# Kernel optimization log

Measured on AMD Instinct MI355X. Metric: run time of the kernel, lower is better.

The kernel has to match this reference:

```python
import jax, jax.numpy as jnp
import numpy as np

B, S, D, H, DK, F, L, V = 4, 128, 512, 8, 64, 2048, 2, 32000
N = B * S  # nodes per side (enc and dec each)


def _pe():
    pos = np.arange(S, dtype=np.float32)[:, None]
    div = np.exp(-np.log(10000.0) * np.arange(0, D, 2, dtype=np.float32) / D)
    pe = np.zeros((S, D), dtype=np.float32)
    pe[:, 0::2] = np.sin(pos * div)
    pe[:, 1::2] = np.cos(pos * div)
    return jnp.asarray(np.tile(pe, (B, 1)))  # [N, D]


def _ln(x, g, b, eps=1e-5):
    mu = jnp.mean(x, -1, keepdims=True)
    var = jnp.mean(jnp.square(x - mu), -1, keepdims=True)
    return g * (x - mu) * jax.lax.rsqrt(var + eps) + b


def _edge_attn(q, k, v, src, dst, n_dst):
    # src_dot_dst('k','q','score') then scaled_exp, then src_mul_edge + sum scatter
    s = jnp.sum(k[src] * q[dst], -1, keepdims=True) / np.float32(np.sqrt(DK))  # [E,H,1]
    s = jnp.exp(jnp.clip(s, -10.0, 10.0))
    wv = jax.ops.segment_sum(v[src] * s, dst, num_segments=n_dst)  # [n_dst,H,DK]
    z = jax.ops.segment_sum(s, dst, num_segments=n_dst)            # [n_dst,H,1]
    return wv / z


def _attn_block(x_q, x_kv, Wq, Wk, Wv, Wo, src, dst):
    q = (x_q @ Wq).reshape(-1, H, DK)
    k = (x_kv @ Wk).reshape(-1, H, DK)
    v = (x_kv @ Wv).reshape(-1, H, DK)
    o = _edge_attn(q, k, v, src, dst, x_q.shape[0]).reshape(-1, D)
    return o @ Wo


def _forward(p, src_tok, tgt_tok, ee_src, ee_dst, dd_src, dd_dst, ed_src, ed_dst):
    (src_emb, tgt_emb, enc_Wqkv, enc_Wo, enc_ln1, enc_W1, enc_b1, enc_W2, enc_b2,
     enc_ln2, enc_lnf, dec_Wqkv, dec_Wo, dec_ln1, dec_cWq, dec_cWkv, dec_cWo,
     dec_ln2, dec_W1, dec_b1, dec_W2, dec_b2, dec_ln3, dec_lnf, gen_W, gen_b) = p
    pe = _pe()
    scale = np.float32(np.sqrt(D))
    x_e = src_emb[src_tok].reshape(N, D) * scale + pe  # token + positional embed
    x_d = tgt_emb[tgt_tok].reshape(N, D) * scale + pe
    for l in range(L):  # encoder layers (ee edges)
        xn = _ln(x_e, enc_ln1[l, 0], enc_ln1[l, 1])
        x_e = x_e + _attn_block(xn, xn, enc_Wqkv[l, 0], enc_Wqkv[l, 1], enc_Wqkv[l, 2], enc_Wo[l], ee_src, ee_dst)
        xn = _ln(x_e, enc_ln2[l, 0], enc_ln2[l, 1])
        x_e = x_e + jax.nn.relu(xn @ enc_W1[l] + enc_b1[l]) @ enc_W2[l] + enc_b2[l]
    x_e = _ln(x_e, enc_lnf[0], enc_lnf[1])
    for l in range(L):  # decoder layers: self (dd) then cross (ed)
        xn = _ln(x_d, dec_ln1[l, 0], dec_ln1[l, 1])
        x_d = x_d + _attn_block(xn, xn, dec_Wqkv[l, 0], dec_Wqkv[l, 1], dec_Wqkv[l, 2], dec_Wo[l], dd_src, dd_dst)
        xn = _ln(x_d, dec_ln2[l, 0], dec_ln2[l, 1])
        x_d = x_d + _attn_block(xn, x_e, dec_cWq[l], dec_cWkv[l, 0], dec_cWkv[l, 1], dec_cWo[l], ed_src, ed_dst)
        xn = _ln(x_d, dec_ln3[l, 0], dec_ln3[l, 1])
        x_d = x_d + jax.nn.relu(xn @ dec_W1[l] + dec_b1[l]) @ dec_W2[l] + dec_b2[l]
    x_d = _ln(x_d, dec_lnf[0], dec_lnf[1])
    return jax.nn.log_softmax(x_d @ gen_W + gen_b, axis=-1)  # generator


def setup_inputs():
    key = jax.random.key(0)
    ks = iter(jax.random.split(key, 32))
    w = lambda *shape: jax.random.normal(next(ks), shape, jnp.float32) * 0.02
    lnp = lambda n: jnp.tile(jnp.stack([jnp.ones(D), jnp.zeros(D)])[None], (n, 1, 1))
    # structured edge lists: per-sentence blocks
    i, j = np.meshgrid(np.arange(S), np.arange(S), indexing='ij')  # src pos, dst pos
    base = (np.arange(B)[:, None] * S).astype(np.int32)
    full_s = (base + i.ravel()[None, :]).ravel().astype(np.int32)
    full_d = (base + j.ravel()[None, :]).ravel().astype(np.int32)
    m = i.ravel() <= j.ravel()  # causal mask for dec self-attention
    dd_s = (base + i.ravel()[m][None, :]).ravel().astype(np.int32)
    dd_d = (base + j.ravel()[m][None, :]).ravel().astype(np.int32)
    k1, k2 = jax.random.split(next(ks))
    return dict(
        src_emb=w(V, D), tgt_emb=w(V, D),
        enc_Wqkv=w(L, 3, D, D), enc_Wo=w(L, D, D), enc_ln1=lnp(L),
        enc_W1=w(L, D, F), enc_b1=jnp.zeros((L, F)), enc_W2=w(L, F, D),
        enc_b2=jnp.zeros((L, D)), enc_ln2=lnp(L), enc_lnf=lnp(1)[0],
        dec_Wqkv=w(L, 3, D, D), dec_Wo=w(L, D, D), dec_ln1=lnp(L),
        dec_cWq=w(L, D, D), dec_cWkv=w(L, 2, D, D), dec_cWo=w(L, D, D), dec_ln2=lnp(L),
        dec_W1=w(L, D, F), dec_b1=jnp.zeros((L, F)), dec_W2=w(L, F, D),
        dec_b2=jnp.zeros((L, D)), dec_ln3=lnp(L), dec_lnf=lnp(1)[0],
        gen_W=w(D, V), gen_b=jnp.zeros((V,)),
        src_tok=jax.random.randint(k1, (B, S), 0, V, jnp.int32),
        tgt_tok=jax.random.randint(k2, (B, S), 0, V, jnp.int32),
        ee_src=jnp.asarray(full_s), ee_dst=jnp.asarray(full_d),
        dd_src=jnp.asarray(dd_s), dd_dst=jnp.asarray(dd_d),
        ed_src=jnp.asarray(full_s), ed_dst=jnp.asarray(full_d),
    )


def reference(src_emb, tgt_emb, enc_Wqkv, enc_Wo, enc_ln1, enc_W1, enc_b1, enc_W2,
              enc_b2, enc_ln2, enc_lnf, dec_Wqkv, dec_Wo, dec_ln1, dec_cWq,
              dec_cWkv, dec_cWo, dec_ln2, dec_W1, dec_b1, dec_W2, dec_b2,
              dec_ln3, dec_lnf, gen_W, gen_b, src_tok, tgt_tok, ee_src, ee_dst,
              dd_src, dd_dst, ed_src, ed_dst):
    p = (src_emb, tgt_emb, enc_Wqkv, enc_Wo, enc_ln1, enc_W1, enc_b1, enc_W2,
         enc_b2, enc_ln2, enc_lnf, dec_Wqkv, dec_Wo, dec_ln1, dec_cWq, dec_cWkv,
         dec_cWo, dec_ln2, dec_W1, dec_b1, dec_W2, dec_b2, dec_ln3, dec_lnf,
         gen_W, gen_b)
    return _forward(p, src_tok, tgt_tok, ee_src, ee_dst, dd_src, dd_dst, ed_src, ed_dst)
```

## Files before the change

### kernel.cpp

```cpp
#include <hip/hip_runtime.h>
#include <cstddef>

constexpr int cB = 4, cS = 128, cD = 512, cH = 8, cDK = 64, cF = 2048, cL = 2, cV = 32000;
constexpr int cN = cB * cS;

typedef __attribute__((ext_vector_type(8)))  short short8;
typedef __attribute__((ext_vector_type(4)))  float f32x4;
typedef __attribute__((ext_vector_type(16))) float f32x16;

__device__ __forceinline__ short f2bf(float x) {
    unsigned u = __builtin_bit_cast(unsigned, x);
    unsigned r = (u + 0x7fffu + ((u >> 16) & 1u)) >> 16;
    return (short)r;
}
__device__ __forceinline__ short f2h(float x) {
    return __builtin_bit_cast(short, (_Float16)x);
}
__device__ __forceinline__ float h2f(short s) {
    return (float)__builtin_bit_cast(_Float16, s);
}

__device__ __forceinline__ void bar_lgkm() {
    asm volatile("s_waitcnt lgkmcnt(0)" ::: "memory");
    __builtin_amdgcn_s_barrier();
    asm volatile("" ::: "memory");
}

__global__ __launch_bounds__(256) void embed_k(const float* __restrict__ e0,
                                               const int* __restrict__ t0,
                                               float* __restrict__ X0,
                                               const float* __restrict__ e1,
                                               const int* __restrict__ t1,
                                               float* __restrict__ X1)
{
    const float* emb = blockIdx.z ? e1 : e0;
    const int* tok   = blockIdx.z ? t1 : t0;
    float* X         = blockIdx.z ? X1 : X0;
    int n = blockIdx.x;
    int tid = threadIdx.x;
    int t = tok[n];
    int pos = n & (cS - 1);
    const float scale = 22.62741699796952f;
    for (int d = tid; d < cD; d += 256) {
        int i2 = d & ~1;
        float div = expf(-9.210340371976184f * (float)i2 / (float)cD);
        float arg = (float)pos * div;
        float p = (d & 1) ? cosf(arg) : sinf(arg);
        X[(long)n * cD + d] = emb[(long)t * cD + d] * scale + p;
    }
}

__global__ __launch_bounds__(256) void ln_k(const float* __restrict__ X,
                                            const float* __restrict__ g,
                                            const float* __restrict__ bta,
                                            short* __restrict__ Yb)
{
    __shared__ float red[256];
    int row = blockIdx.x, tid = threadIdx.x;
    const float* x = X + (long)row * cD;
    float v0 = x[tid], v1 = x[tid + 256];

    red[tid] = v0 + v1;
    __syncthreads();
    for (int st = 128; st > 0; st >>= 1) { if (tid < st) red[tid] += red[tid + st]; __syncthreads(); }
    float mu = red[0] * (1.0f / (float)cD);
    __syncthreads();

    float d0 = v0 - mu, d1 = v1 - mu;
    red[tid] = d0 * d0 + d1 * d1;
    __syncthreads();
    for (int st = 128; st > 0; st >>= 1) { if (tid < st) red[tid] += red[tid + st]; __syncthreads(); }
    float var = red[0] * (1.0f / (float)cD);
    float rs = rsqrtf(var + 1e-5f);

    Yb[(long)row * cD + tid]       = f2bf(g[tid]       * d0 * rs + bta[tid]);
    Yb[(long)row * cD + tid + 256] = f2bf(g[tid + 256] * d1 * rs + bta[tid + 256]);
}

struct TCP { const float* s[24]; };

__global__ __launch_bounds__(256) void tconv_k(TCP ptrs, short* __restrict__ dst,
                                               int K, int N)
{
    __shared__ float t[64][65];
    const float* s = ptrs.s[blockIdx.z];
    short* d = dst + (long)blockIdx.z * K * N;
    int k0 = blockIdx.y * 64, n0 = blockIdx.x * 64;
    int tid = threadIdx.x;
    const f32x4* s4 = (const f32x4*)s;
#pragma unroll
    for (int i = 0; i < 4; i++) {
        int lin = tid + i * 256;
        int r = lin >> 4, c4 = lin & 15;
        f32x4 v = s4[(long)(k0 + r) * (N >> 2) + (n0 >> 2) + c4];
        t[r][c4 * 4 + 0] = v[0]; t[r][c4 * 4 + 1] = v[1];
        t[r][c4 * 4 + 2] = v[2]; t[r][c4 * 4 + 3] = v[3];
    }
    __syncthreads();
#pragma unroll
    for (int i = 0; i < 2; i++) {
        int lin = tid + i * 256;
        int r = lin >> 3, c8 = lin & 7;
        short8 o;
#pragma unroll
        for (int j = 0; j < 8; j++) o[j] = f2bf(t[c8 * 8 + j][r]);
        *(short8*)&d[(long)(n0 + r) * K + k0 + c8 * 8] = o;
    }
}

template <int MR, int NR, bool LNF>
__global__ __launch_bounds__(256) void gemm_k(
    const short* __restrict__ Abf, const float* __restrict__ Af,
    const float* __restrict__ lng, const float* __restrict__ lnb,
    const short* __restrict__ Bt,
    const float* __restrict__ bias, const float* __restrict__ res,
    float* __restrict__ C, short* __restrict__ Cb,
    int N, int K, int relu, long btStride, long cStride, int swz)
{
    constexpr int BM = MR * 32, BN = NR * 32, BK = 64, PITCH = BK + 8;
    constexpr int ACH = (BM * BK) / (8 * 256);
    constexpr int BCH = (BN * BK) / (8 * 256);
    static_assert(ACH >= 1 && BCH >= 1, "tile too small");
    __shared__ short As[2][BM * PITCH];
    __shared__ short Bs[2][BN * PITCH];
    __shared__ float mu_s[BM], rs_s[BM];
    __shared__ float gb_s[2][512];

    int bx = blockIdx.x, by = blockIdx.y;
    if (swz) {
        int nb = gridDim.x * gridDim.y;
        int bid = by * gridDim.x + bx;
        int w = (bid & 7) * (nb >> 3) + (bid >> 3);
        by = w % gridDim.y; bx = w / gridDim.y;
    }

    const short* Bm = Bt + (long)blockIdx.z * btStride;
    int tid = threadIdx.x;
    int lane = tid & 63, wid = tid >> 6;
    int wr = wid >> 1, wc = wid & 1;
    int m0 = by * BM, n0 = bx * BN;
    int lrow = lane & 15, koff = (lane >> 4) * 8;

    f32x4 acc[MR][NR];
#pragma unroll
    for (int m = 0; m < MR; m++)
#pragma unroll
        for (int n = 0; n < NR; n++) acc[m][n] = f32x4{0.f, 0.f, 0.f, 0.f};

    short8 qa0[ACH], qa1[ACH], qb0[BCH], qb1[BCH];
    f32x4 fa0[LNF ? ACH * 2 : 1], fa1[LNF ? ACH * 2 : 1];

    auto stageA = [&](int k0, short8 (&qa)[ACH], f32x4 (&fa)[LNF ? ACH * 2 : 1]) {
#pragma unroll
        for (int i = 0; i < ACH; i++) {
            int lin = tid + i * 256, r = lin >> 3, c8 = lin & 7;
            if constexpr (LNF) {
                const f32x4* p = (const f32x4*)(Af + (long)(m0 + r) * K + k0 + c8 * 8);
                fa[2 * i] = p[0]; fa[2 * i + 1] = p[1];
            } else {
                qa[i] = *(const short8*)&Abf[(long)(m0 + r) * K + k0 + c8 * 8];
            }
        }
    };
    auto stageB = [&](int k0, short8 (&qb)[BCH]) {
#pragma unroll
        for (int i = 0; i < BCH; i++) {
            int lin = tid + i * 256, r = lin >> 3, c8 = lin & 7;
            qb[i] = *(const short8*)&Bm[(long)(n0 + r) * K + k0 + c8 * 8];
        }
    };
    auto writeT = [&](int buf, int k0, short8 (&qa)[ACH],
                      f32x4 (&fa)[LNF ? ACH * 2 : 1], short8 (&qb)[BCH]) {
#pragma unroll
        for (int i = 0; i < ACH; i++) {
            int lin = tid + i * 256, r = lin >> 3, c8 = lin & 7;
            if constexpr (LNF) {
                float mu = mu_s[r], rs = rs_s[r];
                short8 o;
#pragma unroll
                for (int j = 0; j < 4; j++)
                    o[j] = f2bf((fa[2 * i][j] - mu) * rs * gb_s[0][k0 + c8 * 8 + j] + gb_s[1][k0 + c8 * 8 + j]);
#pragma unroll
                for (int j = 0; j < 4; j++)
                    o[4 + j] = f2bf((fa[2 * i + 1][j] - mu) * rs * gb_s[0][k0 + c8 * 8 + 4 + j] + gb_s[1][k0 + c8 * 8 + 4 + j]);
                *(short8*)&As[buf][r * PITCH + c8 * 8] = o;
            } else {
                *(short8*)&As[buf][r * PITCH + c8 * 8] = qa[i];
            }
        }
#pragma unroll
        for (int i = 0; i < BCH; i++) {
            int lin = tid + i * 256, r = lin >> 3, c8 = lin & 7;
            *(short8*)&Bs[buf][r * PITCH + c8 * 8] = qb[i];
        }
    };
    auto mfmaStep = [&](int buf) {
#pragma unroll
        for (int kk = 0; kk < BK; kk += 32) {
            short8 a[MR], b[NR];
#pragma unroll
            for (int m = 0; m < MR; m++)
                a[m] = *(const short8*)&As[buf][(wr * MR * 16 + m * 16 + lrow) * PITCH + kk + koff];
#pragma unroll
            for (int n = 0; n < NR; n++)
                b[n] = *(const short8*)&Bs[buf][(wc * NR * 16 + n * 16 + lrow) * PITCH + kk + koff];
#pragma unroll
            for (int m = 0; m < MR; m++)
#pragma unroll
                for (int n = 0; n < NR; n++)
                    acc[m][n] = __builtin_amdgcn_mfma_f32_16x16x32_bf16(a[m], b[n], acc[m][n], 0, 0, 0);
        }
    };

    stageA(0, qa0, fa0); stageB(0, qb0);
    if (BK < K) { stageA(BK, qa1, fa1); stageB(BK, qb1); }

    if constexpr (LNF) {
        constexpr int TPR = 256 / BM;
        int r = tid / TPR, sub = tid % TPR;
        const f32x4* row4 = (const f32x4*)(Af + (long)(m0 + r) * K);
        float s = 0.f, s2 = 0.f;
        for (int i = sub; i < (K >> 2); i += TPR) {
            f32x4 v = row4[i];
            s  += v[0] + v[1] + v[2] + v[3];
            s2 += v[0] * v[0] + v[1] * v[1] + v[2] * v[2] + v[3] * v[3];
        }
#pragma unroll
        for (int o = TPR >> 1; o > 0; o >>= 1) {
            s += __shfl_xor(s, o); s2 += __shfl_xor(s2, o);
        }
        if (sub == 0) {
            float mu = s / (float)K;
            float var = s2 / (float)K - mu * mu;
            mu_s[r] = mu; rs_s[r] = rsqrtf(var + 1e-5f);
        }
        for (int i = tid; i < 512; i += 256) {
            gb_s[0][i] = lng[i]; gb_s[1][i] = lnb[i];
        }
        bar_lgkm();
    }

    int k0 = 0;
    for (;;) {
        writeT(0, k0, qa0, fa0, qb0);
        if (k0 + 2 * BK < K) { stageA(k0 + 2 * BK, qa0, fa0); stageB(k0 + 2 * BK, qb0); }
        bar_lgkm();
        mfmaStep(0);
        k0 += BK; if (k0 >= K) break;

        writeT(1, k0, qa1, fa1, qb1);
        if (k0 + 2 * BK < K) { stageA(k0 + 2 * BK, qa1, fa1); stageB(k0 + 2 * BK, qb1); }
        bar_lgkm();
        mfmaStep(1);
        k0 += BK; if (k0 >= K) break;
    }

#pragma unroll
    for (int m = 0; m < MR; m++) {
        int rbase = m0 + wr * MR * 16 + m * 16 + (lane >> 4) * 4;
#pragma unroll
        for (int n = 0; n < NR; n++) {
            int col = n0 + wc * NR * 16 + n * 16 + (lane & 15);
            float bv = bias ? bias[col] : 0.f;
#pragma unroll
            for (int j = 0; j < 4; j++) {
                long row = rbase + j;
                float v = acc[m][n][j] + bv;
                if (res)  v += res[row * N + col];
                if (relu) v = fmaxf(v, 0.f);
                long off = row * N + col + (long)blockIdx.z * cStride;
                if (C)  C[off] = v;
                if (Cb) Cb[off] = f2bf(v);
            }
        }
    }
}

__global__ __launch_bounds__(256) void attn_k(const short* __restrict__ Q,
                                              const short* __restrict__ Km,
                                              const short* __restrict__ Vm,
                                              short* __restrict__ O, int causal)
{
    __shared__ short q_s[64 * 72];
    __shared__ short k_s[128 * 72];
    __shared__ short vt_s[64 * 128];
    __shared__ short p_s[64 * 136];
    __shared__ float z_s[64];

    int tid = threadIdx.x, lane = tid & 63, wid = tid >> 6;
    int lr = lane & 15, lg = lane >> 4;
    int h = blockIdx.x, b = blockIdx.y, dstBase = blockIdx.z * 64;
    const int RS = cH * cDK;
    long qbase = ((long)b * cS + dstBase) * RS + h * cDK;
    long kbase = ((long)b * cS) * RS + h * cDK;

#pragma unroll
    for (int i = 0; i < 2; i++) {
        int lin = tid + i * 256, t = lin >> 3, c8 = lin & 7;
        *(short8*)&q_s[t * 72 + c8 * 8] = *(const short8*)&Q[qbase + (long)t * RS + c8 * 8];
    }
#pragma unroll
    for (int i = 0; i < 4; i++) {
        int lin = tid + i * 256, t = lin >> 3, c8 = lin & 7;
        *(short8*)&k_s[t * 72 + c8 * 8] = *(const short8*)&Km[kbase + (long)t * RS + c8 * 8];
    }
#pragma unroll
    for (int i = 0; i < 4; i++) {
        int lin = tid + i * 256, src = lin >> 3, c8 = lin & 7;
        short8 v = *(const short8*)&Vm[kbase + (long)src * RS + c8 * 8];
#pragma unroll
        for (int j = 0; j < 8; j++) {
            int dk = c8 * 8 + j;
            int g = (src >> 3) ^ (dk >> 3);
            vt_s[dk * 128 + g * 8 + (src & 7)] = v[j];
        }
    }
    bar_lgkm();

    f32x4 sacc[8];
#pragma unroll
    for (int n = 0; n < 8; n++) sacc[n] = f32x4{0.f, 0.f, 0.f, 0.f};
#pragma unroll
    for (int kk = 0; kk < 64; kk += 32) {
        short8 a = *(const short8*)&q_s[(wid * 16 + lr) * 72 + kk + lg * 8];
#pragma unroll
        for (int n = 0; n < 8; n++) {
            short8 bf = *(const short8*)&k_s[(n * 16 + lr) * 72 + kk + lg * 8];
            sacc[n] = __builtin_amdgcn_mfma_f32_16x16x32_bf16(a, bf, sacc[n], 0, 0, 0);
        }
    }
    float z[4] = {0.f, 0.f, 0.f, 0.f};
#pragma unroll
    for (int n = 0; n < 8; n++) {
        int src = n * 16 + lr;
#pragma unroll
        for (int j = 0; j < 4; j++) {
            int dst = dstBase + wid * 16 + lg * 4 + j;
            float s = sacc[n][j] * 0.125f;
            s = __expf(fminf(fmaxf(s, -10.f), 10.f));
            if (causal && src > dst) s = 0.f;
            sacc[n][j] = s;
            z[j] += s;
        }
    }
#pragma unroll
    for (int j = 0; j < 4; j++) {
        z[j] += __shfl_xor(z[j], 1); z[j] += __shfl_xor(z[j], 2);
        z[j] += __shfl_xor(z[j], 4); z[j] += __shfl_xor(z[j], 8);
    }
#pragma unroll
    for (int n = 0; n < 8; n++) {
        int src = n * 16 + lr;
#pragma unroll
        for (int j = 0; j < 4; j++)
            p_s[(wid * 16 + lg * 4 + j) * 136 + src] = f2bf(sacc[n][j]);
    }
    if (lr == 0) {
#pragma unroll
        for (int j = 0; j < 4; j++) z_s[wid * 16 + lg * 4 + j] = z[j];
    }
    bar_lgkm();

    f32x4 oacc[4];
#pragma unroll
    for (int n = 0; n < 4; n++) oacc[n] = f32x4{0.f, 0.f, 0.f, 0.f};
#pragma unroll
    for (int kk = 0; kk < 128; kk += 32) {
        int dkr = wid * 16 + lr;
        int g = ((kk >> 3) + lg) ^ (dkr >> 3);
        short8 a = *(const short8*)&vt_s[dkr * 128 + g * 8];
#pragma unroll
        for (int n = 0; n < 4; n++) {
            short8 bf = *(const short8*)&p_s[(n * 16 + lr) * 136 + kk + lg * 8];
            oacc[n] = __builtin_amdgcn_mfma_f32_16x16x32_bf16(a, bf, oacc[n], 0, 0, 0);
        }
    }
#pragma unroll
    for (int n = 0; n < 4; n++) {
        int dl = n * 16 + lr;
        float zz = z_s[dl];
#pragma unroll
        for (int j = 0; j < 4; j++) {
            int dk = wid * 16 + lg * 4 + j;
            O[qbase + (long)dl * RS + dk] = f2bf(oacc[n][j] / zz);
        }
    }
}

__global__ __launch_bounds__(256) void gen32_k(
    const short* __restrict__ A, const short* __restrict__ Bt,
    const float* __restrict__ bias, short* __restrict__ Ch, int N, int K)
{
    constexpr int PITCH = 72;
    constexpr int ACH = 4, BCH = 4;
    __shared__ short As[2][128 * PITCH];
    __shared__ short Bs[2][128 * PITCH];

    int bx = blockIdx.x, by = blockIdx.y;
    {
        int nb = gridDim.x * gridDim.y;
        int bid = by * gridDim.x + bx;
        int w = (bid & 7) * (nb >> 3) + (bid >> 3);
        by = w % gridDim.y; bx = w / gridDim.y;
    }
    int tid = threadIdx.x;
    int lane = tid & 63, wid = tid >> 6;
    int wr = wid >> 1, wc = wid & 1;
    int m0 = by * 128, n0 = bx * 128;
    int l31 = lane & 31, l5 = lane >> 5;

    f32x16 acc[2][2];
#pragma unroll
    for (int m = 0; m < 2; m++)
#pragma unroll
        for (int n = 0; n < 2; n++)
#pragma unroll
            for (int r = 0; r < 16; r++) acc[m][n][r] = 0.f;

    short8 qa0[ACH], qa1[ACH], qb0[BCH], qb1[BCH];
    auto stage = [&](int k0, short8 (&qa)[ACH], short8 (&qb)[BCH]) {
#pragma unroll
        for (int i = 0; i < ACH; i++) {
            int lin = tid + i * 256, r = lin >> 3, c8 = lin & 7;
            qa[i] = *(const short8*)&A[(long)(m0 + r) * K + k0 + c8 * 8];
        }
#pragma unroll
        for (int i = 0; i < BCH; i++) {
            int lin = tid + i * 256, r = lin >> 3, c8 = lin & 7;
            qb[i] = *(const short8*)&Bt[(long)(n0 + r) * K + k0 + c8 * 8];
        }
    };
    auto writeT = [&](int buf, short8 (&qa)[ACH], short8 (&qb)[BCH]) {
#pragma unroll
        for (int i = 0; i < ACH; i++) {
            int lin = tid + i * 256, r = lin >> 3, c8 = lin & 7;
            *(short8*)&As[buf][r * PITCH + c8 * 8] = qa[i];
        }
#pragma unroll
        for (int i = 0; i < BCH; i++) {
            int lin = tid + i * 256, r = lin >> 3, c8 = lin & 7;
            *(short8*)&Bs[buf][r * PITCH + c8 * 8] = qb[i];
        }
    };
    auto mfmaStep = [&](int buf) {
#pragma unroll
        for (int kk = 0; kk < 64; kk += 16) {
            short8 a[2], b[2];
#pragma unroll
            for (int m = 0; m < 2; m++)
                a[m] = *(const short8*)&As[buf][(wr * 64 + m * 32 + l31) * PITCH + kk + l5 * 8];
#pragma unroll
            for (int n = 0; n < 2; n++)
                b[n] = *(const short8*)&Bs[buf][(wc * 64 + n * 32 + l31) * PITCH + kk + l5 * 8];
#pragma unroll
            for (int m = 0; m < 2; m++)
#pragma unroll
                for (int n = 0; n < 2; n++)
                    acc[m][n] = __builtin_amdgcn_mfma_f32_32x32x16_bf16(a[m], b[n], acc[m][n], 0, 0, 0);
        }
    };

    const int steps = K >> 6;
    stage(0, qa0, qb0);
    stage(64, qa1, qb1);
    int st = 0;
    for (;;) {
        writeT(0, qa0, qb0);
        if (st + 2 < steps) stage((st + 2) * 64, qa0, qb0);
        bar_lgkm();
        mfmaStep(0);
        st++; if (st >= steps) break;

        writeT(1, qa1, qb1);
        if (st + 2 < steps) stage((st + 2) * 64, qa1, qb1);
        bar_lgkm();
        mfmaStep(1);
        st++; if (st >= steps) break;
    }

#pragma unroll
    for (int m = 0; m < 2; m++) {
#pragma unroll
        for (int n = 0; n < 2; n++) {
            int col = n0 + wc * 64 + n * 32 + l31;
            float bv = bias[col];
#pragma unroll
            for (int r = 0; r < 16; r++) {
                int row = m0 + wr * 64 + m * 32 + (r & 3) + 8 * (r >> 2) + 4 * l5;
                Ch[(long)row * N + col] = f2h(acc[m][n][r] + bv);
            }
        }
    }
}

__global__ __launch_bounds__(256) void lsm_k(const short* __restrict__ L16,
                                             float* __restrict__ Out)
{
    __shared__ float rm[256], rs[256];
    int row = blockIdx.x, tid = threadIdx.x;
    const short8* x8 = (const short8*)(L16 + (long)row * cV);
    float* o = Out + (long)row * cV;
    constexpr int NV = cV / 8;

    float m = -1e30f, s = 0.f;
    for (int i = tid; i < NV; i += 256) {
        short8 v = x8[i];
        float f[8];
#pragma unroll
        for (int j = 0; j < 8; j++) f[j] = h2f(v[j]);
        float cm = f[0];
#pragma unroll
        for (int j = 1; j < 8; j++) cm = fmaxf(cm, f[j]);
        float nm = fmaxf(m, cm);
        float a = 0.f;
#pragma unroll
        for (int j = 0; j < 8; j++) a += __expf(f[j] - nm);
        s = s * __expf(m - nm) + a;
        m = nm;
    }
    rm[tid] = m; rs[tid] = s;
    __syncthreads();
    for (int st = 128; st > 0; st >>= 1) {
        if (tid < st) {
            float m2 = rm[tid + st], s2 = rs[tid + st];
            float nm = fmaxf(rm[tid], m2);
            rs[tid] = rs[tid] * __expf(rm[tid] - nm) + s2 * __expf(m2 - nm);
            rm[tid] = nm;
        }
        __syncthreads();
    }
    float lse = rm[0] + __logf(rs[0]);

    for (int i = tid; i < NV; i += 256) {
        short8 v = x8[i];
        f32x4 o0, o1;
#pragma unroll
        for (int j = 0; j < 4; j++) o0[j] = h2f(v[j]) - lse;
#pragma unroll
        for (int j = 0; j < 4; j++) o1[j] = h2f(v[4 + j]) - lse;
        *(f32x4*)&o[i * 8]     = o0;
        *(f32x4*)&o[i * 8 + 4] = o1;
    }
}

extern "C" void kernel_launch(void* const* d_in, const int* in_sizes, int n_in,
                              void* d_out, int out_size, void* d_ws, size_t ws_size,
                              hipStream_t stream)
{
    const float* src_emb  = (const float*)d_in[0];
    const float* tgt_emb  = (const float*)d_in[1];
    const float* enc_Wqkv = (const float*)d_in[2];
    const float* enc_Wo   = (const float*)d_in[3];
    const float* enc_ln1  = (const float*)d_in[4];
    const float* enc_W1   = (const float*)d_in[5];
    const float* enc_b1   = (const float*)d_in[6];
    const float* enc_W2   = (const float*)d_in[7];
    const float* enc_b2   = (const float*)d_in[8];
    const float* enc_ln2  = (const float*)d_in[9];
    const float* enc_lnf  = (const float*)d_in[10];
    const float* dec_Wqkv = (const float*)d_in[11];
    const float* dec_Wo   = (const float*)d_in[12];
    const float* dec_ln1  = (const float*)d_in[13];
    const float* dec_cWq  = (const float*)d_in[14];
    const float* dec_cWkv = (const float*)d_in[15];
    const float* dec_cWo  = (const float*)d_in[16];
    const float* dec_ln2  = (const float*)d_in[17];
    const float* dec_W1   = (const float*)d_in[18];
    const float* dec_b1   = (const float*)d_in[19];
    const float* dec_W2   = (const float*)d_in[20];
    const float* dec_b2   = (const float*)d_in[21];
    const float* dec_ln3  = (const float*)d_in[22];
    const float* dec_lnf  = (const float*)d_in[23];
    const float* gen_W    = (const float*)d_in[24];
    const float* gen_b    = (const float*)d_in[25];
    const int* src_tok    = (const int*)d_in[26];
    const int* tgt_tok    = (const int*)d_in[27];

    const long ND = (long)cN * cD;
    const long DD = (long)cD * cD;
    const long DF = (long)cD * cF;

    float* x_e = (float*)d_ws;
    float* x_d = x_e + ND;

    short* qkvb  = (short*)(x_d + ND);
    short* ob_bf = qkvb + 3 * ND;
    short* hb_bf = ob_bf + ND;
    short* kvc   = hb_bf + (long)cN * cF;
    short* xn_bf = kvc + 4 * ND;
    short* wDD  = xn_bf + ND;
    short* wDF  = wDD + 24 * DD;
    short* wFD  = wDF + 4 * DF;
    short* genT = wFD + 4 * DF;
    short* lg16 = genT + (long)cD * cV;

    {
        TCP p{};
        int i = 0;
        for (int j = 0; j < 6; j++) p.s[i++] = enc_Wqkv + (long)j * DD;
        for (int j = 0; j < 2; j++) p.s[i++] = enc_Wo   + (long)j * DD;
        for (int j = 0; j < 6; j++) p.s[i++] = dec_Wqkv + (long)j * DD;
        for (int j = 0; j < 2; j++) p.s[i++] = dec_Wo   + (long)j * DD;
        for (int j = 0; j < 2; j++) p.s[i++] = dec_cWq  + (long)j * DD;
        for (int j = 0; j < 4; j++) p.s[i++] = dec_cWkv + (long)j * DD;
        for (int j = 0; j < 2; j++) p.s[i++] = dec_cWo  + (long)j * DD;
        tconv_k<<<dim3(cD / 64, cD / 64, 24), 256, 0, stream>>>(p, wDD, cD, cD);
    }
    {
        TCP p{};
        p.s[0] = enc_W1; p.s[1] = enc_W1 + DF; p.s[2] = dec_W1; p.s[3] = dec_W1 + DF;
        tconv_k<<<dim3(cF / 64, cD / 64, 4), 256, 0, stream>>>(p, wDF, cD, cF);
    }
    {
        TCP p{};
        p.s[0] = enc_W2; p.s[1] = enc_W2 + DF; p.s[2] = dec_W2; p.s[3] = dec_W2 + DF;
        tconv_k<<<dim3(cD / 64, cF / 64, 4), 256, 0, stream>>>(p, wFD, cF, cD);
    }
    {
        TCP p{};
        p.s[0] = gen_W;
        tconv_k<<<dim3(cV / 64, cD / 64, 1), 256, 0, stream>>>(p, genT, cD, cV);
    }

    embed_k<<<dim3(cN, 1, 2), 256, 0, stream>>>(src_emb, src_tok, x_e,
                                                tgt_emb, tgt_tok, x_d);

    dim3 gDD(cD / 32, cN / 32);
    dim3 gFFN1(cF / 64, cN / 64);
    dim3 gAttn(cH, cB, 2);

    for (int l = 0; l < cL; l++) {
        gemm_k<1, 1, true><<<dim3(cD / 32, cN / 32, 3), 256, 0, stream>>>(
            nullptr, x_e, enc_ln1 + (long)(2 * l) * cD, enc_ln1 + (long)(2 * l + 1) * cD,
            wDD + (long)(3 * l) * DD, nullptr, nullptr, nullptr, qkvb,
            cD, cD, 0, DD, ND, 0);
        attn_k<<<gAttn, 256, 0, stream>>>(qkvb, qkvb + ND, qkvb + 2 * ND, ob_bf, 0);
        gemm_k<1, 1, false><<<gDD, 256, 0, stream>>>(
            ob_bf, nullptr, nullptr, nullptr, wDD + (long)(6 + l) * DD,
            nullptr, x_e, x_e, nullptr, cD, cD, 0, 0, 0, 0);
        gemm_k<2, 2, true><<<gFFN1, 256, 0, stream>>>(
            nullptr, x_e, enc_ln2 + (long)(2 * l) * cD, enc_ln2 + (long)(2 * l + 1) * cD,
            wDF + (long)l * DF, enc_b1 + (long)l * cF, nullptr, nullptr, hb_bf,
            cF, cD, 1, 0, 0, 0);
        gemm_k<1, 1, false><<<gDD, 256, 0, stream>>>(
            hb_bf, nullptr, nullptr, nullptr, wFD + (long)l * DF,
            enc_b2 + (long)l * cD, x_e, x_e, nullptr, cD, cF, 0, 0, 0, 0);
    }

    gemm_k<1, 1, true><<<dim3(cD / 32, cN / 32, 4), 256, 0, stream>>>(
        nullptr, x_e, enc_lnf, enc_lnf + cD,
        wDD + 18 * DD, nullptr, nullptr, nullptr, kvc, cD, cD, 0, DD, ND, 0);

    for (int l = 0; l < cL; l++) {
        gemm_k<1, 1, true><<<dim3(cD / 32, cN / 32, 3), 256, 0, stream>>>(
            nullptr, x_d, dec_ln1 + (long)(2 * l) * cD, dec_ln1 + (long)(2 * l + 1) * cD,
            wDD + (long)(8 + 3 * l) * DD, nullptr, nullptr, nullptr, qkvb,
            cD, cD, 0, DD, ND, 0);
        attn_k<<<gAttn, 256, 0, stream>>>(qkvb, qkvb + ND, qkvb + 2 * ND, ob_bf, 1);
        gemm_k<1, 1, false><<<gDD, 256, 0, stream>>>(
            ob_bf, nullptr, nullptr, nullptr, wDD + (long)(14 + l) * DD,
            nullptr, x_d, x_d, nullptr, cD, cD, 0, 0, 0, 0);

        gemm_k<1, 1, true><<<gDD, 256, 0, stream>>>(
            nullptr, x_d, dec_ln2 + (long)(2 * l) * cD, dec_ln2 + (long)(2 * l + 1) * cD,
            wDD + (long)(16 + l) * DD, nullptr, nullptr, nullptr, qkvb,
            cD, cD, 0, 0, 0, 0);
        attn_k<<<gAttn, 256, 0, stream>>>(qkvb, kvc + (long)(2 * l) * ND,
                                          kvc + (long)(2 * l + 1) * ND, ob_bf, 0);
        gemm_k<1, 1, false><<<gDD, 256, 0, stream>>>(
            ob_bf, nullptr, nullptr, nullptr, wDD + (long)(22 + l) * DD,
            nullptr, x_d, x_d, nullptr, cD, cD, 0, 0, 0, 0);

        gemm_k<2, 2, true><<<gFFN1, 256, 0, stream>>>(
            nullptr, x_d, dec_ln3 + (long)(2 * l) * cD, dec_ln3 + (long)(2 * l + 1) * cD,
            wDF + (long)(2 + l) * DF, dec_b1 + (long)l * cF, nullptr, nullptr, hb_bf,
            cF, cD, 1, 0, 0, 0);
        gemm_k<1, 1, false><<<gDD, 256, 0, stream>>>(
            hb_bf, nullptr, nullptr, nullptr, wFD + (long)(2 + l) * DF,
            dec_b2 + (long)l * cD, x_d, x_d, nullptr, cD, cF, 0, 0, 0, 0);
    }

    ln_k<<<cN, 256, 0, stream>>>(x_d, dec_lnf, dec_lnf + cD, xn_bf);
    gen32_k<<<dim3(cV / 128, cN / 128), 256, 0, stream>>>(
        xn_bf, genT, gen_b, lg16, cV, cD);
    lsm_k<<<cN, 256, 0, stream>>>(lg16, (float*)d_out);
}
```

Before: 357.0 us.

## Split K across two warp groups in 512-thread GEMM with shared-memory reduction

Replaces the 256-thread layer GEMM with a 512-thread variant in which two groups of four warps each handle half of the K dimension, staging 128-wide K slices. The two partial accumulators are combined through shared memory before the epilogue. LayerNorm normalisation now happens in registers when the tile is staged rather than when it is written to LDS, and the grid swizzle option is removed. The vocabulary GEMM also drops from a K tile of 64 to 32, which halves its LDS footprint but doubles its barrier steps. The aim is more warps per block to hide latency on these small GEMMs, at the cost of an extra reduction pass and more barriers.

```diff
diff --git a/kernel.cpp b/kernel.cpp
--- a/kernel.cpp
+++ b/kernel.cpp
@@ -109,114 +109,35 @@
 }
 
 template <int MR, int NR, bool LNF>
-__global__ __launch_bounds__(256) void gemm_k(
+__global__ __launch_bounds__(512) void gemm8_k(
     const short* __restrict__ Abf, const float* __restrict__ Af,
     const float* __restrict__ lng, const float* __restrict__ lnb,
     const short* __restrict__ Bt,
     const float* __restrict__ bias, const float* __restrict__ res,
     float* __restrict__ C, short* __restrict__ Cb,
-    int N, int K, int relu, long btStride, long cStride, int swz)
-{
-    constexpr int BM = MR * 32, BN = NR * 32, BK = 64, PITCH = BK + 8;
-    constexpr int ACH = (BM * BK) / (8 * 256);
-    constexpr int BCH = (BN * BK) / (8 * 256);
+    int N, int K, int relu, long btStride, long cStride)
+{
+    constexpr int BM = MR * 32, BN = NR * 32, PITCH = 136;
+    constexpr int ACH = (BM * 128) / (8 * 512);
+    constexpr int BCH = (BN * 128) / (8 * 512);
     static_assert(ACH >= 1 && BCH >= 1, "tile too small");
     __shared__ short As[2][BM * PITCH];
     __shared__ short Bs[2][BN * PITCH];
+    __shared__ float red[4][64][MR * NR * 4];
     __shared__ float mu_s[BM], rs_s[BM];
-    __shared__ float gb_s[2][512];
-
-    int bx = blockIdx.x, by = blockIdx.y;
-    if (swz) {
-        int nb = gridDim.x * gridDim.y;
-        int bid = by * gridDim.x + bx;
-        int w = (bid & 7) * (nb >> 3) + (bid >> 3);
-        by = w % gridDim.y; bx = w / gridDim.y;
-    }
+    __shared__ float gb_s[2][LNF ? 512 : 8];
 
     const short* Bm = Bt + (long)blockIdx.z * btStride;
     int tid = threadIdx.x;
     int lane = tid & 63, wid = tid >> 6;
-    int wr = wid >> 1, wc = wid & 1;
-    int m0 = by * BM, n0 = bx * BN;
+    int grp = wid >> 2, quad = wid & 3;
+    int wr = quad >> 1, wc = quad & 1;
+    int m0 = blockIdx.y * BM, n0 = blockIdx.x * BN;
     int lrow = lane & 15, koff = (lane >> 4) * 8;
-
-    f32x4 acc[MR][NR];
-#pragma unroll
-    for (int m = 0; m < MR; m++)
-#pragma unroll
-        for (int n = 0; n < NR; n++) acc[m][n] = f32x4{0.f, 0.f, 0.f, 0.f};
-
-    short8 qa0[ACH], qa1[ACH], qb0[BCH], qb1[BCH];
-    f32x4 fa0[LNF ? ACH * 2 : 1], fa1[LNF ? ACH * 2 : 1];
-
-    auto stageA = [&](int k0, short8 (&qa)[ACH], f32x4 (&fa)[LNF ? ACH * 2 : 1]) {
-#pragma unroll
-        for (int i = 0; i < ACH; i++) {
-            int lin = tid + i * 256, r = lin >> 3, c8 = lin & 7;
-            if constexpr (LNF) {
-                const f32x4* p = (const f32x4*)(Af + (long)(m0 + r) * K + k0 + c8 * 8);
-                fa[2 * i] = p[0]; fa[2 * i + 1] = p[1];
-            } else {
-                qa[i] = *(const short8*)&Abf[(long)(m0 + r) * K + k0 + c8 * 8];
-            }
-        }
-    };
-    auto stageB = [&](int k0, short8 (&qb)[BCH]) {
-#pragma unroll
-        for (int i = 0; i < BCH; i++) {
-            int lin = tid + i * 256, r = lin >> 3, c8 = lin & 7;
-            qb[i] = *(const short8*)&Bm[(long)(n0 + r) * K + k0 + c8 * 8];
-        }
-    };
-    auto writeT = [&](int buf, int k0, short8 (&qa)[ACH],
-                      f32x4 (&fa)[LNF ? ACH * 2 : 1], short8 (&qb)[BCH]) {
-#pragma unroll
-        for (int i = 0; i < ACH; i++) {
-            int lin = tid + i * 256, r = lin >> 3, c8 = lin & 7;
-            if constexpr (LNF) {
-                float mu = mu_s[r], rs = rs_s[r];
-                short8 o;
-#pragma unroll
-                for (int j = 0; j < 4; j++)
-                    o[j] = f2bf((fa[2 * i][j] - mu) * rs * gb_s[0][k0 + c8 * 8 + j] + gb_s[1][k0 + c8 * 8 + j]);
-#pragma unroll
-                for (int j = 0; j < 4; j++)
-                    o[4 + j] = f2bf((fa[2 * i + 1][j] - mu) * rs * gb_s[0][k0 + c8 * 8 + 4 + j] + gb_s[1][k0 + c8 * 8 + 4 + j]);
-                *(short8*)&As[buf][r * PITCH + c8 * 8] = o;
-            } else {
-                *(short8*)&As[buf][r * PITCH + c8 * 8] = qa[i];
-            }
-        }
-#pragma unroll
-        for (int i = 0; i < BCH; i++) {
-            int lin = tid + i * 256, r = lin >> 3, c8 = lin & 7;
-            *(short8*)&Bs[buf][r * PITCH + c8 * 8] = qb[i];
-        }
-    };
-    auto mfmaStep = [&](int buf) {
-#pragma unroll
-        for (int kk = 0; kk < BK; kk += 32) {
-            short8 a[MR], b[NR];
-#pragma unroll
-            for (int m = 0; m < MR; m++)
-                a[m] = *(const short8*)&As[buf][(wr * MR * 16 + m * 16 + lrow) * PITCH + kk + koff];
-#pragma unroll
-            for (int n = 0; n < NR; n++)
-                b[n] = *(const short8*)&Bs[buf][(wc * NR * 16 + n * 16 + lrow) * PITCH + kk + koff];
-#pragma unroll
-            for (int m = 0; m < MR; m++)
-#pragma unroll
-                for (int n = 0; n < NR; n++)
-                    acc[m][n] = __builtin_amdgcn_mfma_f32_16x16x32_bf16(a[m], b[n], acc[m][n], 0, 0, 0);
-        }
-    };
-
-    stageA(0, qa0, fa0); stageB(0, qb0);
-    if (BK < K) { stageA(BK, qa1, fa1); stageB(BK, qb1); }
+    const int Kh = K >> 1;
 
     if constexpr (LNF) {
-        constexpr int TPR = 256 / BM;
+        constexpr int TPR = 512 / BM;
         int r = tid / TPR, sub = tid % TPR;
         const f32x4* row4 = (const f32x4*)(Af + (long)(m0 + r) * K);
         float s = 0.f, s2 = 0.f;
@@ -234,43 +155,125 @@
             float var = s2 / (float)K - mu * mu;
             mu_s[r] = mu; rs_s[r] = rsqrtf(var + 1e-5f);
         }
-        for (int i = tid; i < 512; i += 256) {
-            gb_s[0][i] = lng[i]; gb_s[1][i] = lnb[i];
-        }
+        if (tid < 512) { gb_s[0][tid] = lng[tid]; gb_s[1][tid] = lnb[tid]; }
         bar_lgkm();
     }
 
-    int k0 = 0;
+    f32x4 acc[MR][NR];
+#pragma unroll
+    for (int m = 0; m < MR; m++)
+#pragma unroll
+        for (int n = 0; n < NR; n++) acc[m][n] = f32x4{0.f, 0.f, 0.f, 0.f};
+
+    short8 qa0[ACH], qa1[ACH], qb0[BCH], qb1[BCH];
+
+    auto stage = [&](int step, short8 (&qa)[ACH], short8 (&qb)[BCH]) {
+#pragma unroll
+        for (int i = 0; i < ACH; i++) {
+            int lin = tid + i * 512, r = lin >> 4, c8 = lin & 15;
+            int kg = (c8 < 8) ? (step * 64 + c8 * 8) : (Kh + step * 64 + (c8 - 8) * 8);
+            if constexpr (LNF) {
+                const f32x4* p = (const f32x4*)(Af + (long)(m0 + r) * K + kg);
+                f32x4 f0 = p[0], f1 = p[1];
+                float mu = mu_s[r], rs = rs_s[r];
+                short8 o;
+#pragma unroll
+                for (int j = 0; j < 4; j++)
+                    o[j] = f2bf((f0[j] - mu) * rs * gb_s[0][kg + j] + gb_s[1][kg + j]);
+#pragma unroll
+                for (int j = 0; j < 4; j++)
+                    o[4 + j] = f2bf((f1[j] - mu) * rs * gb_s[0][kg + 4 + j] + gb_s[1][kg + 4 + j]);
+                qa[i] = o;
+            } else {
+                qa[i] = *(const short8*)&Abf[(long)(m0 + r) * K + kg];
+            }
+        }
+#pragma unroll
+        for (int i = 0; i < BCH; i++) {
+            int lin = tid + i * 512, r = lin >> 4, c8 = lin & 15;
+            int kg = (c8 < 8) ? (step * 64 + c8 * 8) : (Kh + step * 64 + (c8 - 8) * 8);
+            qb[i] = *(const short8*)&Bm[(long)(n0 + r) * K + kg];
+        }
+    };
+    auto writeT = [&](int buf, short8 (&qa)[ACH], short8 (&qb)[BCH]) {
+#pragma unroll
+        for (int i = 0; i < ACH; i++) {
+            int lin = tid + i * 512, r = lin >> 4, c8 = lin & 15;
+            *(short8*)&As[buf][r * PITCH + c8 * 8] = qa[i];
+        }
+#pragma unroll
+        for (int i = 0; i < BCH; i++) {
+            int lin = tid + i * 512, r = lin >> 4, c8 = lin & 15;
+            *(short8*)&Bs[buf][r * PITCH + c8 * 8] = qb[i];
+        }
+    };
+    auto mfmaStep = [&](int buf) {
+#pragma unroll
+        for (int kk2 = 0; kk2 < 2; kk2++) {
+            int kk = grp * 64 + kk2 * 32;
+            short8 a[MR], b[NR];
+#pragma unroll
+            for (int m = 0; m < MR; m++)
+                a[m] = *(const short8*)&As[buf][(wr * MR * 16 + m * 16 + lrow) * PITCH + kk + koff];
+#pragma unroll
+            for (int n = 0; n < NR; n++)
+                b[n] = *(const short8*)&Bs[buf][(wc * NR * 16 + n * 16 + lrow) * PITCH + kk + koff];
+#pragma unroll
+            for (int m = 0; m < MR; m++)
+#pragma unroll
+                for (int n = 0; n < NR; n++)
+                    acc[m][n] = __builtin_amdgcn_mfma_f32_16x16x32_bf16(a[m], b[n], acc[m][n], 0, 0, 0);
+        }
+    };
+
+    const int steps = K >> 7;
+    stage(0, qa0, qb0);
+    if (steps > 1) stage(1, qa1, qb1);
+
+    int st = 0;
     for (;;) {
-        writeT(0, k0, qa0, fa0, qb0);
-        if (k0 + 2 * BK < K) { stageA(k0 + 2 * BK, qa0, fa0); stageB(k0 + 2 * BK, qb0); }
+        writeT(0, qa0, qb0);
+        if (st + 2 < steps) stage(st + 2, qa0, qb0);
         bar_lgkm();
         mfmaStep(0);
-        k0 += BK; if (k0 >= K) break;
-
-        writeT(1, k0, qa1, fa1, qb1);
-        if (k0 + 2 * BK < K) { stageA(k0 + 2 * BK, qa1, fa1); stageB(k0 + 2 * BK, qb1); }
+        st++; if (st >= steps) break;
+
+        writeT(1, qa1, qb1);
+        if (st + 2 < steps) stage(st + 2, qa1, qb1);
         bar_lgkm();
         mfmaStep(1);
-        k0 += BK; if (k0 >= K) break;
-    }
-
-#pragma unroll
-    for (int m = 0; m < MR; m++) {
-        int rbase = m0 + wr * MR * 16 + m * 16 + (lane >> 4) * 4;
-#pragma unroll
-        for (int n = 0; n < NR; n++) {
-            int col = n0 + wc * NR * 16 + n * 16 + (lane & 15);
-            float bv = bias ? bias[col] : 0.f;
-#pragma unroll
-            for (int j = 0; j < 4; j++) {
-                long row = rbase + j;
-                float v = acc[m][n][j] + bv;
-                if (res)  v += res[row * N + col];
-                if (relu) v = fmaxf(v, 0.f);
-                long off = row * N + col + (long)blockIdx.z * cStride;
-                if (C)  C[off] = v;
-                if (Cb) Cb[off] = f2bf(v);
+        st++; if (st >= steps) break;
+    }
+
+    __syncthreads();
+    if (grp == 1) {
+#pragma unroll
+        for (int m = 0; m < MR; m++)
+#pragma unroll
+            for (int n = 0; n < NR; n++)
+#pragma unroll
+                for (int j = 0; j < 4; j++)
+                    red[quad][lane][(m * NR + n) * 4 + j] = acc[m][n][j];
+    }
+    __syncthreads();
+    if (grp == 0) {
+#pragma unroll
+        for (int m = 0; m < MR; m++) {
+            int rbase = m0 + wr * MR * 16 + m * 16 + (lane >> 4) * 4;
+#pragma unroll
+            for (int n = 0; n < NR; n++) {
+                int col = n0 + wc * NR * 16 + n * 16 + (lane & 15);
+                float bv = bias ? bias[col] : 0.f;
+#pragma unroll
+                for (int j = 0; j < 4; j++) {
+                    long row = rbase + j;
+                    float v = acc[m][n][j] + red[quad][lane][(m * NR + n) * 4 + j] + bv;
+                    if (res)  v += res[row * N + col];
+                    if (relu) v = fmaxf(v, 0.f);
+                    long off = row * N + col + (long)blockIdx.z * cStride;
+                    if (C)  C[off] = v;
+                    if (Cb) Cb[off] = f2bf(v);
+                }
             }
         }
     }
@@ -391,8 +394,8 @@
     const short* __restrict__ A, const short* __restrict__ Bt,
     const float* __restrict__ bias, short* __restrict__ Ch, int N, int K)
 {
-    constexpr int PITCH = 72;
-    constexpr int ACH = 4, BCH = 4;
+    constexpr int PITCH = 40;
+    constexpr int ACH = 2, BCH = 2;
     __shared__ short As[2][128 * PITCH];
     __shared__ short Bs[2][128 * PITCH];
 
@@ -421,30 +424,30 @@
     auto stage = [&](int k0, short8 (&qa)[ACH], short8 (&qb)[BCH]) {
 #pragma unroll
         for (int i = 0; i < ACH; i++) {
-            int lin = tid + i * 256, r = lin >> 3, c8 = lin & 7;
+            int lin = tid + i * 256, r = lin >> 2, c8 = lin & 3;
             qa[i] = *(const short8*)&A[(long)(m0 + r) * K + k0 + c8 * 8];
         }
 #pragma unroll
         for (int i = 0; i < BCH; i++) {
-            int lin = tid + i * 256, r = lin >> 3, c8 = lin & 7;
+            int lin = tid + i * 256, r = lin >> 2, c8 = lin & 3;
             qb[i] = *(const short8*)&Bt[(long)(n0 + r) * K + k0 + c8 * 8];
         }
     };
     auto writeT = [&](int buf, short8 (&qa)[ACH], short8 (&qb)[BCH]) {
 #pragma unroll
         for (int i = 0; i < ACH; i++) {
-            int lin = tid + i * 256, r = lin >> 3, c8 = lin & 7;
+            int lin = tid + i * 256, r = lin >> 2, c8 = lin & 3;
             *(short8*)&As[buf][r * PITCH + c8 * 8] = qa[i];
         }
 #pragma unroll
         for (int i = 0; i < BCH; i++) {
-            int lin = tid + i * 256, r = lin >> 3, c8 = lin & 7;
+            int lin = tid + i * 256, r = lin >> 2, c8 = lin & 3;
             *(short8*)&Bs[buf][r * PITCH + c8 * 8] = qb[i];
         }
     };
     auto mfmaStep = [&](int buf) {
 #pragma unroll
-        for (int kk = 0; kk < 64; kk += 16) {
+        for (int kk = 0; kk < 32; kk += 16) {
             short8 a[2], b[2];
 #pragma unroll
             for (int m = 0; m < 2; m++)
@@ -460,19 +463,19 @@
         }
     };
 
-    const int steps = K >> 6;
+    const int steps = K >> 5;
     stage(0, qa0, qb0);
-    stage(64, qa1, qb1);
+    stage(32, qa1, qb1);
     int st = 0;
     for (;;) {
         writeT(0, qa0, qb0);
-        if (st + 2 < steps) stage((st + 2) * 64, qa0, qb0);
+        if (st + 2 < steps) stage((st + 2) * 32, qa0, qb0);
         bar_lgkm();
         mfmaStep(0);
         st++; if (st >= steps) break;
 
         writeT(1, qa1, qb1);
-        if (st + 2 < steps) stage((st + 2) * 64, qa1, qb1);
+        if (st + 2 < steps) stage((st + 2) * 32, qa1, qb1);
         bar_lgkm();
         mfmaStep(1);
         st++; if (st >= steps) break;
@@ -630,54 +633,54 @@
     dim3 gAttn(cH, cB, 2);
 
     for (int l = 0; l < cL; l++) {
-        gemm_k<1, 1, true><<<dim3(cD / 32, cN / 32, 3), 256, 0, stream>>>(
+        gemm8_k<1, 1, true><<<dim3(cD / 32, cN / 32, 3), 512, 0, stream>>>(
             nullptr, x_e, enc_ln1 + (long)(2 * l) * cD, enc_ln1 + (long)(2 * l + 1) * cD,
             wDD + (long)(3 * l) * DD, nullptr, nullptr, nullptr, qkvb,
-            cD, cD, 0, DD, ND, 0);
+            cD, cD, 0, DD, ND);
         attn_k<<<gAttn, 256, 0, stream>>>(qkvb, qkvb + ND, qkvb + 2 * ND, ob_bf, 0);
-        gemm_k<1, 1, false><<<gDD, 256, 0, stream>>>(
+        gemm8_k<1, 1, false><<<gDD, 512, 0, stream>>>(
             ob_bf, nullptr, nullptr, nullptr, wDD + (long)(6 + l) * DD,
-            nullptr, x_e, x_e, nullptr, cD, cD, 0, 0, 0, 0);
-        gemm_k<2, 2, true><<<gFFN1, 256, 0, stream>>>(
+            nullptr, x_e, x_e, nullptr, cD, cD, 0, 0, 0);
+        gemm8_k<2, 2, true><<<gFFN1, 512, 0, stream>>>(
             nullptr, x_e, enc_ln2 + (long)(2 * l) * cD, enc_ln2 + (long)(2 * l + 1) * cD,
             wDF + (long)l * DF, enc_b1 + (long)l * cF, nullptr, nullptr, hb_bf,
-            cF, cD, 1, 0, 0, 0);
-        gemm_k<1, 1, false><<<gDD, 256, 0, stream>>>(
+            cF, cD, 1, 0, 0);
+        gemm8_k<1, 1, false><<<gDD, 512, 0, stream>>>(
             hb_bf, nullptr, nullptr, nullptr, wFD + (long)l * DF,
-            enc_b2 + (long)l * cD, x_e, x_e, nullptr, cD, cF, 0, 0, 0, 0);
-    }
-
-    gemm_k<1, 1, true><<<dim3(cD / 32, cN / 32, 4), 256, 0, stream>>>(
+            enc_b2 + (long)l * cD, x_e, x_e, nullptr, cD, cF, 0, 0, 0);
+    }
+
+    gemm8_k<1, 1, true><<<dim3(cD / 32, cN / 32, 4), 512, 0, stream>>>(
         nullptr, x_e, enc_lnf, enc_lnf + cD,
-        wDD + 18 * DD, nullptr, nullptr, nullptr, kvc, cD, cD, 0, DD, ND, 0);
+        wDD + 18 * DD, nullptr, nullptr, nullptr, kvc, cD, cD, 0, DD, ND);
 
     for (int l = 0; l < cL; l++) {
-        gemm_k<1, 1, true><<<dim3(cD / 32, cN / 32, 3), 256, 0, stream>>>(
+        gemm8_k<1, 1, true><<<dim3(cD / 32, cN / 32, 3), 512, 0, stream>>>(
             nullptr, x_d, dec_ln1 + (long)(2 * l) * cD, dec_ln1 + (long)(2 * l + 1) * cD,
             wDD + (long)(8 + 3 * l) * DD, nullptr, nullptr, nullptr, qkvb,
-            cD, cD, 0, DD, ND, 0);
+            cD, cD, 0, DD, ND);
         attn_k<<<gAttn, 256, 0, stream>>>(qkvb, qkvb + ND, qkvb + 2 * ND, ob_bf, 1);
-        gemm_k<1, 1, false><<<gDD, 256, 0, stream>>>(
+        gemm8_k<1, 1, false><<<gDD, 512, 0, stream>>>(
             ob_bf, nullptr, nullptr, nullptr, wDD + (long)(14 + l) * DD,
-            nullptr, x_d, x_d, nullptr, cD, cD, 0, 0, 0, 0);
-
-        gemm_k<1, 1, true><<<gDD, 256, 0, stream>>>(
+            nullptr, x_d, x_d, nullptr, cD, cD, 0, 0, 0);
+
+        gemm8_k<1, 1, true><<<gDD, 512, 0, stream>>>(
             nullptr, x_d, dec_ln2 + (long)(2 * l) * cD, dec_ln2 + (long)(2 * l + 1) * cD,
             wDD + (long)(16 + l) * DD, nullptr, nullptr, nullptr, qkvb,
-            cD, cD, 0, 0, 0, 0);
+            cD, cD, 0, 0, 0);
         attn_k<<<gAttn, 256, 0, stream>>>(qkvb, kvc + (long)(2 * l) * ND,
                                           kvc + (long)(2 * l + 1) * ND, ob_bf, 0);
-        gemm_k<1, 1, false><<<gDD, 256, 0, stream>>>(
+        gemm8_k<1, 1, false><<<gDD, 512, 0, stream>>>(
             ob_bf, nullptr, nullptr, nullptr, wDD + (long)(22 + l) * DD,
-            nullptr, x_d, x_d, nullptr, cD, cD, 0, 0, 0, 0);
-
-        gemm_k<2, 2, true><<<gFFN1, 256, 0, stream>>>(
+            nullptr, x_d, x_d, nullptr, cD, cD, 0, 0, 0);
+
+        gemm8_k<2, 2, true><<<gFFN1, 512, 0, stream>>>(
             nullptr, x_d, dec_ln3 + (long)(2 * l) * cD, dec_ln3 + (long)(2 * l + 1) * cD,
             wDF + (long)(2 + l) * DF, dec_b1 + (long)l * cF, nullptr, nullptr, hb_bf,
-            cF, cD, 1, 0, 0, 0);
-        gemm_k<1, 1, false><<<gDD, 256, 0, stream>>>(
+            cF, cD, 1, 0, 0);
+        gemm8_k<1, 1, false><<<gDD, 512, 0, stream>>>(
             hb_bf, nullptr, nullptr, nullptr, wFD + (long)(2 + l) * DF,
-            dec_b2 + (long)l * cD, x_d, x_d, nullptr, cD, cF, 0, 0, 0, 0);
+            dec_b2 + (long)l * cD, x_d, x_d, nullptr, cD, cF, 0, 0, 0);
     }
 
     ln_k<<<cN, 256, 0, stream>>>(x_d, dec_lnf, dec_lnf + cD, xn_bf);
```

Result: no change. 355.5 us (-0.4%).
